# Performance work log

Measured on AMD Instinct MI355X. Metric: run time of the kernel, lower is better.

The kernel has to match this reference:

```python
import jax, jax.numpy as jnp
import numpy as np

N_RAYS, N_SAMPLES = 131072, 128
FAR_DELTA = 1e9  # sentinel delta for the last sample, as in the torch source


def setup_inputs() -> dict:
    key = jax.random.key(0)
    k1, k2 = jax.random.split(key)
    # rgbo: [N, S, 4] raw network outputs; channels 0:3 raw rgb, channel 3 density.
    # Density drawn from U[0,1) so transmittance exponentials stay bounded.
    rgbo = jax.random.uniform(k1, (N_RAYS, N_SAMPLES, 4), dtype=jnp.float32)
    # depth: [N, S] sorted sample depths along each ray (near=2.0, far=6.0).
    depth = jnp.sort(
        jax.random.uniform(k2, (N_RAYS, N_SAMPLES), dtype=jnp.float32,
                           minval=2.0, maxval=6.0), axis=1)
    return {"rgbo": rgbo, "depth": depth}


def reference(rgbo, depth):
    # Volumetric alpha-compositing (NeRF.render)
    rgb_normed = jax.nn.sigmoid(rgbo[..., :3])          # [N, S, 3]
    opacity = rgbo[..., 3]                               # [N, S]
    far = jnp.full((depth.shape[0], 1), FAR_DELTA, dtype=depth.dtype)
    delta = jnp.concatenate([depth[:, 1:] - depth[:, :-1], far], axis=1)  # [N, S]
    mult = -opacity * delta                              # [N, S]
    # transmittance T_i = exp(sum_{j<i} -sigma_j * delta_j), exclusive scan
    ts = jnp.exp(jnp.concatenate(
        [jnp.zeros_like(mult[:, :1]), jnp.cumsum(mult, axis=1)[:, :-1]], axis=1))
    alpha = 1.0 - jnp.exp(mult)                          # [N, S]
    weights = ts * alpha                                 # [N, S]
    # weighted reduction over depth samples -> composited color per ray
    return jnp.sum(weights[..., None] * rgb_normed, axis=1)  # [N, 3]
```

## Files before the change

kernel.cpp:

```cpp
#include <hip/hip_runtime.h>


#define NERF_N_SAMPLES 128
#define NERF_FAR_DELTA 1e9f

__device__ __forceinline__ float sigmoidf_fast(float x) {
    return 1.0f / (1.0f + __expf(-x));
}

__global__ __launch_bounds__(256) void nerf_render_kernel(
    const float4* __restrict__ rgbo,
    const float*  __restrict__ depth,
    float*        __restrict__ out,
    int n_rays)
{
    const int gtid = blockIdx.x * blockDim.x + threadIdx.x;
    const int ray  = gtid >> 6;
    const int lane = threadIdx.x & 63;
    if (ray >= n_rays) return;

    const float4* rbase = rgbo + (size_t)ray * NERF_N_SAMPLES;
    const float4 ra = rbase[lane];
    const float4 rb = rbase[lane + 64];

    const float* dbase = depth + (size_t)ray * NERF_N_SAMPLES;
    const float da = dbase[lane];
    const float db = dbase[lane + 64];

    const float da_next = __shfl_down(da, 1, 64);
    const float db_next = __shfl_down(db, 1, 64);
    const float d64     = __shfl(db, 0, 64);

    const float delta_a = (lane == 63) ? (d64 - da)      : (da_next - da);
    const float delta_b = (lane == 63) ? NERF_FAR_DELTA  : (db_next - db);

    const float m_a = -ra.w * delta_a;
    const float m_b = -rb.w * delta_b;

    float sa = m_a;
    #pragma unroll
    for (int off = 1; off < 64; off <<= 1) {
        float y = __shfl_up(sa, off, 64);
        if (lane >= off) sa += y;
    }
    float sb = m_b;
    #pragma unroll
    for (int off = 1; off < 64; off <<= 1) {
        float y = __shfl_up(sb, off, 64);
        if (lane >= off) sb += y;
    }

    const float excl_a_raw = __shfl_up(sa, 1, 64);
    const float excl_b_raw = __shfl_up(sb, 1, 64);
    const float excl_a = (lane == 0) ? 0.0f : excl_a_raw;
    const float total_a = __shfl(sa, 63, 64);
    const float excl_b = total_a + ((lane == 0) ? 0.0f : excl_b_raw);

    const float w_a = __expf(excl_a) - __expf(excl_a + m_a);
    const float w_b = __expf(excl_b) - __expf(excl_b + m_b);

    float c0 = w_a * sigmoidf_fast(ra.x) + w_b * sigmoidf_fast(rb.x);
    float c1 = w_a * sigmoidf_fast(ra.y) + w_b * sigmoidf_fast(rb.y);
    float c2 = w_a * sigmoidf_fast(ra.z) + w_b * sigmoidf_fast(rb.z);

    #pragma unroll
    for (int off = 32; off > 0; off >>= 1) {
        c0 += __shfl_xor(c0, off, 64);
        c1 += __shfl_xor(c1, off, 64);
        c2 += __shfl_xor(c2, off, 64);
    }

    if (lane == 0) {
        float* o = out + (size_t)ray * 3;
        o[0] = c0;
        o[1] = c1;
        o[2] = c2;
    }
}

extern "C" void kernel_launch(void* const* d_in, const int* in_sizes, int n_in,
                              void* d_out, int out_size, void* d_ws, size_t ws_size,
                              hipStream_t stream) {
    const long long s0 = in_sizes[0];
    const long long s1 = in_sizes[1];

    const float4* rgbo;
    const float*  depth;
    long long depth_elems;
    if (s0 >= 4 * s1) {
        rgbo  = (const float4*)d_in[0];
        depth = (const float*)d_in[1];
        depth_elems = s1;
    } else {
        rgbo  = (const float4*)d_in[1];
        depth = (const float*)d_in[0];
        depth_elems = s0;
    }
    const int n_rays = (int)(depth_elems / NERF_N_SAMPLES);

    float* out = (float*)d_out;

    const int block = 256;
    const int rays_per_block = block / 64;
    const int grid = (n_rays + rays_per_block - 1) / rays_per_block;

    nerf_render_kernel<<<grid, block, 0, stream>>>(rgbo, depth, out, n_rays);
}
```

Before: 67.20 us.

## Give each lane two adjacent samples to halve the wavefront scan work

Each lane now owns two consecutive samples instead of samples lane and lane+64. That lets it add the pair locally, run a single 64-lane scan instead of two, share the middle exponential between the two weights, and read depth with one float2 load. The sigmoid division becomes a hardware reciprocal, and the three output channels are written by three lanes in parallel. The strided float4 loads (2*lane) give a different coalescing pattern, and the reciprocal is slightly less precise than a true division.

New measurement: 59.13 us. 1.14x faster.

```diff
diff --git a/kernel.cpp b/kernel.cpp
--- a/kernel.cpp
+++ b/kernel.cpp
@@ -4,8 +4,12 @@
 #define NERF_N_SAMPLES 128
 #define NERF_FAR_DELTA 1e9f
 
+__device__ __forceinline__ float fast_rcp(float x) {
+    return __builtin_amdgcn_rcpf(x);
+}
+
 __device__ __forceinline__ float sigmoidf_fast(float x) {
-    return 1.0f / (1.0f + __expf(-x));
+    return fast_rcp(1.0f + __expf(-x));
 }
 
 __global__ __launch_bounds__(256) void nerf_render_kernel(
@@ -20,48 +24,40 @@
     if (ray >= n_rays) return;
 
     const float4* rbase = rgbo + (size_t)ray * NERF_N_SAMPLES;
-    const float4 ra = rbase[lane];
-    const float4 rb = rbase[lane + 64];
+    const float4 r0 = rbase[2 * lane];
+    const float4 r1 = rbase[2 * lane + 1];
 
-    const float* dbase = depth + (size_t)ray * NERF_N_SAMPLES;
-    const float da = dbase[lane];
-    const float db = dbase[lane + 64];
+    const float2 d = *reinterpret_cast<const float2*>(
+        depth + (size_t)ray * NERF_N_SAMPLES + 2 * lane);
 
-    const float da_next = __shfl_down(da, 1, 64);
-    const float db_next = __shfl_down(db, 1, 64);
-    const float d64     = __shfl(db, 0, 64);
+    const float d_next = __shfl_down(d.x, 1, 64);
+    const float delta0 = d.y - d.x;
+    const float delta1 = (lane == 63) ? NERF_FAR_DELTA : (d_next - d.y);
 
-    const float delta_a = (lane == 63) ? (d64 - da)      : (da_next - da);
-    const float delta_b = (lane == 63) ? NERF_FAR_DELTA  : (db_next - db);
+    const float m0 = -r0.w * delta0;
+    const float m1 = -r1.w * delta1;
+    const float mp = m0 + m1;
 
-    const float m_a = -ra.w * delta_a;
-    const float m_b = -rb.w * delta_b;
-
-    float sa = m_a;
+    float s = mp;
     #pragma unroll
     for (int off = 1; off < 64; off <<= 1) {
-        float y = __shfl_up(sa, off, 64);
-        if (lane >= off) sa += y;
-    }
-    float sb = m_b;
-    #pragma unroll
-    for (int off = 1; off < 64; off <<= 1) {
-        float y = __shfl_up(sb, off, 64);
-        if (lane >= off) sb += y;
+        float y = __shfl_up(s, off, 64);
+        s += (lane >= off) ? y : 0.0f;
     }
 
-    const float excl_a_raw = __shfl_up(sa, 1, 64);
-    const float excl_b_raw = __shfl_up(sb, 1, 64);
-    const float excl_a = (lane == 0) ? 0.0f : excl_a_raw;
-    const float total_a = __shfl(sa, 63, 64);
-    const float excl_b = total_a + ((lane == 0) ? 0.0f : excl_b_raw);
+    const float excl_raw = __shfl_up(s, 1, 64);
+    const float P0 = (lane == 0) ? 0.0f : excl_raw;
+    const float P1 = P0 + m0;
 
-    const float w_a = __expf(excl_a) - __expf(excl_a + m_a);
-    const float w_b = __expf(excl_b) - __expf(excl_b + m_b);
+    const float T0 = __expf(P0);
+    const float T1 = __expf(P1);
+    const float T2 = __expf(P1 + m1);
+    const float w0 = T0 - T1;
+    const float w1 = T1 - T2;
 
-    float c0 = w_a * sigmoidf_fast(ra.x) + w_b * sigmoidf_fast(rb.x);
-    float c1 = w_a * sigmoidf_fast(ra.y) + w_b * sigmoidf_fast(rb.y);
-    float c2 = w_a * sigmoidf_fast(ra.z) + w_b * sigmoidf_fast(rb.z);
+    float c0 = w0 * sigmoidf_fast(r0.x) + w1 * sigmoidf_fast(r1.x);
+    float c1 = w0 * sigmoidf_fast(r0.y) + w1 * sigmoidf_fast(r1.y);
+    float c2 = w0 * sigmoidf_fast(r0.z) + w1 * sigmoidf_fast(r1.z);
 
     #pragma unroll
     for (int off = 32; off > 0; off >>= 1) {
@@ -70,11 +66,9 @@
         c2 += __shfl_xor(c2, off, 64);
     }
 
-    if (lane == 0) {
-        float* o = out + (size_t)ray * 3;
-        o[0] = c0;
-        o[1] = c1;
-        o[2] = c2;
+    if (lane < 3) {
+        const float v = (lane == 0) ? c0 : (lane == 1) ? c1 : c2;
+        out[(size_t)ray * 3 + lane] = v;
     }
 }
 
```
